# Performance work log

Hardware: AMD Instinct MI355X
Metric: run time of the kernel (lower is better)

The kernel has to match this reference:

```python
import jax, jax.numpy as jnp
import numpy as np

B, L, H, W = 4, 5000, 256, 256
C_IN, DIM_LOI, N_PTS0, N_PTS1, DIM_FC, N_OUT_LINE = 256, 128, 32, 8, 1024, 2500
SCALE = N_PTS0 // N_PTS1  # MaxPool1d kernel/stride


def setup_inputs() -> dict:
    key = jax.random.key(0)
    ks = jax.random.split(key, 8)
    feature = jax.random.normal(ks[0], (B, C_IN, H, W), jnp.float32)
    # line endpoints in pixel coords of the 256x256 feature map
    lines = jax.random.uniform(ks[1], (B, L, 2, 2), jnp.float32) * (H - 1)
    s = lambda fan: 1.0 / np.sqrt(fan)
    fc1_w = (jax.random.normal(ks[2], (DIM_LOI, C_IN), jnp.float32) * s(C_IN))
    fc1_b = jnp.zeros((DIM_LOI,), jnp.float32)
    w1 = jax.random.normal(ks[3], (DIM_LOI * N_PTS1, DIM_FC), jnp.float32) * s(DIM_LOI * N_PTS1)
    b1 = jnp.zeros((DIM_FC,), jnp.float32)
    w2 = jax.random.normal(ks[4], (DIM_FC, DIM_FC), jnp.float32) * s(DIM_FC)
    b2 = jnp.zeros((DIM_FC,), jnp.float32)
    w3 = jax.random.normal(ks[5], (DIM_FC, 4), jnp.float32) * s(DIM_FC)
    b3 = jnp.zeros((4,), jnp.float32)
    return dict(feature=feature, lines=lines, fc1_w=fc1_w, fc1_b=fc1_b,
                w1=w1, b1=b1, w2=w2, b2=b2, w3=w3, b3=b3)


def reference(feature, lines, fc1_w, fc1_b, w1, b1, w2, b2, w3, b3):
    # fc1: 1x1 conv  [B,C_IN,H,W] -> [B,DIM_LOI,H,W]
    x = jnp.einsum('bchw,oc->bohw', feature, fc1_w) + fc1_b[None, :, None, None]

    # sample N_PTS0 points along each line (lerp between endpoints), minus 0.5
    lam = jnp.linspace(0.0, 1.0, N_PTS0, dtype=feature.dtype)[None, None, :, None]
    p = lines[:, :, 0:1, :] * lam + lines[:, :, 1:2, :] * (1.0 - lam) - 0.5  # [B,L,P,2]
    px, py = p[..., 0], p[..., 1]  # px indexes H (rows), py indexes W (cols)
    px0 = jnp.clip(jnp.floor(px), 0.0, H - 1.0)
    py0 = jnp.clip(jnp.floor(py), 0.0, W - 1.0)
    px1 = jnp.clip(px0 + 1.0, 0.0, H - 1.0)
    py1 = jnp.clip(py0 + 1.0, 0.0, W - 1.0)
    ix0, iy0 = px0.astype(jnp.int32), py0.astype(jnp.int32)
    ix1, iy1 = px1.astype(jnp.int32), py1.astype(jnp.int32)
    idx00 = ix0 * W + iy0
    idx10 = ix1 * W + iy0
    idx01 = ix0 * W + iy1
    idx11 = ix1 * W + iy1
    w00 = (px1 - px) * (py1 - py)
    w10 = (px - px0) * (py1 - py)
    w01 = (px1 - px) * (py - py0)
    w11 = (px - px0) * (py - py0)

    def gather_one(fmap, i00, i10, i01, i11, g00, g10, g01, g11):
        f = fmap.reshape(DIM_LOI, H * W)
        g = lambda idx: f[:, idx.reshape(-1)].reshape(DIM_LOI, L, N_PTS0)
        return g(i00) * g00 + g(i10) * g10 + g(i01) * g01 + g(i11) * g11

    xp = jax.vmap(gather_one)(x, idx00, idx10, idx01, idx11, w00, w10, w01, w11)
    # xp: [B, DIM_LOI, L, N_PTS0] -> maxpool along points -> [B, DIM_LOI, L, N_PTS1]
    xp = xp.reshape(B, DIM_LOI, L, N_PTS1, SCALE).max(-1)
    # reshape like torch: [N, DIM_LOI, N_PTS1] -> [N, DIM_LOI*N_PTS1] (channel-major)
    feat = xp.transpose(0, 2, 1, 3).reshape(B, L, DIM_LOI * N_PTS1)

    # fc2 MLP -> 4 logits
    h = jax.nn.relu(feat @ w1 + b1)
    h = jax.nn.relu(h @ w2 + b2)
    logits = h @ w3 + b3  # [B, L, 4]
    s = jax.nn.softmax(logits, axis=-1)

    # threshold conditions
    keep = ((s[..., 1] > 0.25) | (s[..., 2] > 0.25) | (s[..., 3] > 0.25)) & (s[..., 0] < 0.25)

    def select(p0, s0, m):
        cnt = m.sum()
        key = jnp.where(m, jnp.argmax(s0, -1), -1)  # masked-out get -1 -> sorted last
        order = jnp.argsort(-key)  # stable desc sort of argmax class
        idx = order[jnp.arange(N_OUT_LINE) % jnp.maximum(cnt, 1)]
        lo = jnp.where(cnt > 0, p0[idx], 0.0)
        so = jnp.where(cnt > 0, s0[idx], 0.0)
        return lo, so

    lines_out, score_out = jax.vmap(select)(lines, s, keep)
    return lines_out, score_out, s
```

## Files before the change

kernel.cpp:

```cpp
#include <hip/hip_runtime.h>
#include <cstdint>
#include <cstddef>

#define B_     4
#define L_     5000
#define H_     256
#define W_     256
#define HW_    65536
#define CIN_   256
#define DLOI_  128
#define NPTS0_ 32
#define NPTS1_ 8
#define DFC_   1024
#define NOUT_  2500
#define M_     (B_*L_)
#define MPAD_  20096
#define NBAND_ 157

typedef _Float16 f16;
typedef _Float16 f16x4 __attribute__((ext_vector_type(4)));
typedef _Float16 f16x8 __attribute__((ext_vector_type(8)));
typedef float    f32x4 __attribute__((ext_vector_type(4)));

__device__ __forceinline__ void gload16(const void* g, void* l) {
  __builtin_amdgcn_global_load_lds(
      (const __attribute__((address_space(1))) void*)g,
      (__attribute__((address_space(3))) void*)l, 16, 0, 0);
}

__global__ __launch_bounds__(256) void k_wsplit(const float* __restrict__ src,
                                                f16* __restrict__ h,
                                                f16* __restrict__ l) {
  int i = (blockIdx.x * 256 + threadIdx.x) * 4;
  float4 v = *(const float4*)(src + i);
  f16 h0 = (f16)v.x, h1 = (f16)v.y, h2 = (f16)v.z, h3 = (f16)v.w;
  *(f16x4*)(h + i) = (f16x4){h0, h1, h2, h3};
  *(f16x4*)(l + i) = (f16x4){(f16)(v.x - (float)h0), (f16)(v.y - (float)h1),
                             (f16)(v.z - (float)h2), (f16)(v.w - (float)h3)};
}

__global__ __launch_bounds__(256) void k_conv_mfma(const float* __restrict__ fin,
                                                   const f16* __restrict__ wh,
                                                   const f16* __restrict__ wl,
                                                   const float* __restrict__ bias,
                                                   float* __restrict__ xout) {
  __shared__ f16 lds[16384];
  const int t = threadIdx.x;
  const int P0 = blockIdx.x * 128;
  const int b  = P0 >> 16;
  const int ph0 = P0 & 65535;
  const int lane = t & 63, wave = t >> 6;
  const int quad = lane >> 4, lo = lane & 15;
  const int wm = wave >> 1, wn = wave & 1;

  const int c_base = (t & 7) * 4;
  const int p = (t >> 3) * 4;
  const size_t fbase = (size_t)b * CIN_ * HW_ + (size_t)ph0 + p;

  const int srow = t >> 2;
  const int skb  = (t & 3) * 16;
  const char* gBh = (const char*)wh + (size_t)srow * 512 + skb;
  const char* gBl = (const char*)wl + (size_t)srow * 512 + skb;
  char* ldsB = (char*)lds + t * 16;

  f32x4 acc[4][4];
  #pragma unroll
  for (int mt = 0; mt < 4; mt++)
    #pragma unroll
    for (int nt = 0; nt < 4; nt++) acc[mt][nt] = (f32x4){0.f, 0.f, 0.f, 0.f};

  float4 av[4], nv[4];
  #pragma unroll
  for (int j = 0; j < 4; j++)
    av[j] = *(const float4*)(fin + fbase + (size_t)(c_base + j) * HW_);

  for (int kc = 0; kc < 8; kc++) {
    const size_t bko = (size_t)kc * 64;
    gload16(gBh + bko,         ldsB + 16384);
    gload16(gBh + 32768 + bko, ldsB + 16384 + 4096);
    gload16(gBl + bko,         ldsB + 24576);
    gload16(gBl + 32768 + bko, ldsB + 24576 + 4096);

    #pragma unroll
    for (int i = 0; i < 4; i++) {
      f16 hh[4], ll[4];
      #pragma unroll
      for (int j = 0; j < 4; j++) {
        float v = ((const float*)&av[j])[i];
        hh[j] = (f16)v;
        ll[j] = (f16)(v - (float)hh[j]);
      }
      *(f16x4*)(&lds[(p + i) * 32 + c_base])        = (f16x4){hh[0], hh[1], hh[2], hh[3]};
      *(f16x4*)(&lds[4096 + (p + i) * 32 + c_base]) = (f16x4){ll[0], ll[1], ll[2], ll[3]};
    }
    __syncthreads();

    if (kc < 7) {
      #pragma unroll
      for (int j = 0; j < 4; j++)
        nv[j] = *(const float4*)(fin + fbase + (size_t)((kc + 1) * 32 + c_base + j) * HW_);
    }

    f16x8 ah[4], al[4], bh4[4], bl4[4];
    #pragma unroll
    for (int mt = 0; mt < 4; mt++) {
      int row = wm * 64 + mt * 16 + lo;
      ah[mt] = *(const f16x8*)(&lds[row * 32 + quad * 8]);
      al[mt] = *(const f16x8*)(&lds[4096 + row * 32 + quad * 8]);
    }
    #pragma unroll
    for (int nt = 0; nt < 4; nt++) {
      int row = wn * 64 + nt * 16 + lo;
      bh4[nt] = *(const f16x8*)(&lds[8192 + row * 32 + quad * 8]);
      bl4[nt] = *(const f16x8*)(&lds[12288 + row * 32 + quad * 8]);
    }
    #pragma unroll
    for (int mt = 0; mt < 4; mt++)
      #pragma unroll
      for (int nt = 0; nt < 4; nt++) {
        acc[mt][nt] = __builtin_amdgcn_mfma_f32_16x16x32_f16(ah[mt], bh4[nt], acc[mt][nt], 0, 0, 0);
        acc[mt][nt] = __builtin_amdgcn_mfma_f32_16x16x32_f16(ah[mt], bl4[nt], acc[mt][nt], 0, 0, 0);
        acc[mt][nt] = __builtin_amdgcn_mfma_f32_16x16x32_f16(al[mt], bh4[nt], acc[mt][nt], 0, 0, 0);
      }
    __syncthreads();
    #pragma unroll
    for (int j = 0; j < 4; j++) av[j] = nv[j];
  }

  #pragma unroll
  for (int nt = 0; nt < 4; nt++) {
    int col = wn * 64 + nt * 16 + lo;
    float bv = bias[col];
    #pragma unroll
    for (int mt = 0; mt < 4; mt++) {
      int rowb = P0 + wm * 64 + mt * 16 + quad * 4;
      #pragma unroll
      for (int r = 0; r < 4; r++)
        xout[(size_t)(rowb + r) * DLOI_ + col] = acc[mt][nt][r] + bv;
    }
  }
}

__global__ __launch_bounds__(128) void k_sample(const float* __restrict__ x,
                                                const float* __restrict__ lines,
                                                f16* __restrict__ fh,
                                                f16* __restrict__ fl) {
  const int blk = blockIdx.x;
  const int b = blk / L_;
  const int c = threadIdx.x;
  const float* ln = lines + (size_t)blk * 4;
  const float e0x = ln[0], e0y = ln[1], e1x = ln[2], e1y = ln[3];
  const float* xb = x + (size_t)b * HW_ * DLOI_;
  f16x8 vh, vl;
  for (int q = 0; q < NPTS1_; q++) {
    float m = -1e30f;
    #pragma unroll
    for (int r = 0; r < 4; r++) {
      int i = q * 4 + r;
      float lam = (float)i * (1.0f / 31.0f);
      float px = e0x * lam + e1x * (1.f - lam) - 0.5f;
      float py = e0y * lam + e1y * (1.f - lam) - 0.5f;
      float px0 = fminf(fmaxf(floorf(px), 0.f), 255.f);
      float py0 = fminf(fmaxf(floorf(py), 0.f), 255.f);
      float px1 = fminf(px0 + 1.f, 255.f);
      float py1 = fminf(py0 + 1.f, 255.f);
      int ix0 = (int)px0, iy0 = (int)py0, ix1 = (int)px1, iy1 = (int)py1;
      float w00 = (px1 - px) * (py1 - py);
      float w10 = (px - px0) * (py1 - py);
      float w01 = (px1 - px) * (py - py0);
      float w11 = (px - px0) * (py - py0);
      float v = w00 * xb[(size_t)(ix0 * W_ + iy0) * DLOI_ + c]
              + w10 * xb[(size_t)(ix1 * W_ + iy0) * DLOI_ + c]
              + w01 * xb[(size_t)(ix0 * W_ + iy1) * DLOI_ + c]
              + w11 * xb[(size_t)(ix1 * W_ + iy1) * DLOI_ + c];
      m = fmaxf(m, v);
    }
    f16 h = (f16)m;
    vh[q] = h;
    vl[q] = (f16)(m - (float)h);
  }
  *(f16x8*)(fh + (size_t)blk * DFC_ + c * 8) = vh;
  *(f16x8*)(fl + (size_t)blk * DFC_ + c * 8) = vl;
}

__global__ __launch_bounds__(256) void k_tsplit(const float* __restrict__ Wsrc,
                                                f16* __restrict__ Th,
                                                f16* __restrict__ Tl) {
  __shared__ float tile[32][33];
  const int bj = blockIdx.x, bi = blockIdx.y;
  const int tx = threadIdx.x & 31, ty = threadIdx.x >> 5;
  #pragma unroll
  for (int r = ty; r < 32; r += 8)
    tile[r][tx] = Wsrc[(size_t)(bi * 32 + r) * 1024 + bj * 32 + tx];
  __syncthreads();
  #pragma unroll
  for (int r = ty; r < 32; r += 8) {
    float v = tile[tx][r];
    f16 h = (f16)v;
    size_t o = (size_t)(bj * 32 + r) * 1024 + bi * 32 + tx;
    Th[o] = h;
    Tl[o] = (f16)(v - (float)h);
  }
}

template <bool SPLIT_OUT>
__global__ __launch_bounds__(256) void k_gemm_f16x3(
    const f16* __restrict__ Ah, const f16* __restrict__ Al,
    const f16* __restrict__ Bh, const f16* __restrict__ Bl,
    const float* __restrict__ bias,
    f16* __restrict__ Oh, f16* __restrict__ Ol,
    const float* __restrict__ w3, float* __restrict__ part) {
  constexpr int K = DFC_;
  __shared__ f16 lds[16384];
  const int bid = blockIdx.x;
  const int xcd = bid & 7;
  const int t8  = bid >> 3;
  const int nb  = t8 & 7;
  const int rb  = xcd * 20 + (t8 >> 3);
  if (rb >= NBAND_) return;
  const int n0 = nb * 128;
  const int r0 = rb * 128;
  const int t = threadIdx.x;
  const int lane = t & 63, wave = t >> 6;
  const int quad = lane >> 4, lo = lane & 15;
  const int wm = wave >> 1, wn = wave & 1;

  const int srow = t >> 2;
  const int skb  = (t & 3) * 16;
  const char* gA_h = (const char*)Ah + (size_t)(r0 + srow) * (K * 2) + skb;
  const char* gA_l = (const char*)Al + (size_t)(r0 + srow) * (K * 2) + skb;
  const char* gB_h = (const char*)Bh + (size_t)(n0 + srow) * (K * 2) + skb;
  const char* gB_l = (const char*)Bl + (size_t)(n0 + srow) * (K * 2) + skb;
  char* lb = (char*)lds + t * 16;
  const size_t rstride64 = (size_t)64 * K * 2;

  f32x4 acc[4][4];
  #pragma unroll
  for (int mt = 0; mt < 4; mt++)
    #pragma unroll
    for (int nt = 0; nt < 4; nt++) acc[mt][nt] = (f32x4){0.f, 0.f, 0.f, 0.f};

  for (int kc = 0; kc < K / 32; kc++) {
    const size_t go = (size_t)kc * 64;
    gload16(gA_h + go,             lb);
    gload16(gA_h + rstride64 + go, lb + 4096);
    gload16(gA_l + go,             lb + 8192);
    gload16(gA_l + rstride64 + go, lb + 12288);
    gload16(gB_h + go,             lb + 16384);
    gload16(gB_h + rstride64 + go, lb + 20480);
    gload16(gB_l + go,             lb + 24576);
    gload16(gB_l + rstride64 + go, lb + 28672);
    __syncthreads();

    f16x8 ah[4], al[4], bh[4], bl[4];
    #pragma unroll
    for (int mt = 0; mt < 4; mt++) {
      int row = wm * 64 + mt * 16 + lo;
      ah[mt] = *(const f16x8*)(lds + row * 32 + quad * 8);
      al[mt] = *(const f16x8*)(lds + 4096 + row * 32 + quad * 8);
    }
    #pragma unroll
    for (int nt = 0; nt < 4; nt++) {
      int row = wn * 64 + nt * 16 + lo;
      bh[nt] = *(const f16x8*)(lds + 8192 + row * 32 + quad * 8);
      bl[nt] = *(const f16x8*)(lds + 12288 + row * 32 + quad * 8);
    }
    #pragma unroll
    for (int mt = 0; mt < 4; mt++)
      #pragma unroll
      for (int nt = 0; nt < 4; nt++) {
        acc[mt][nt] = __builtin_amdgcn_mfma_f32_16x16x32_f16(ah[mt], bh[nt], acc[mt][nt], 0, 0, 0);
        acc[mt][nt] = __builtin_amdgcn_mfma_f32_16x16x32_f16(ah[mt], bl[nt], acc[mt][nt], 0, 0, 0);
        acc[mt][nt] = __builtin_amdgcn_mfma_f32_16x16x32_f16(al[mt], bh[nt], acc[mt][nt], 0, 0, 0);
      }
    __syncthreads();
  }

  if (SPLIT_OUT) {
    #pragma unroll
    for (int mt = 0; mt < 4; mt++)
      #pragma unroll
      for (int nt = 0; nt < 4; nt++) {
        int col = n0 + wn * 64 + nt * 16 + lo;
        float bv = bias[col];
        int rowb = r0 + wm * 64 + mt * 16 + quad * 4;
        #pragma unroll
        for (int r = 0; r < 4; r++) {
          int row = rowb + r;
          if (row < M_) {
            float v = fmaxf(acc[mt][nt][r] + bv, 0.f);
            f16 h = (f16)v;
            Oh[(size_t)row * DFC_ + col] = h;
            Ol[(size_t)row * DFC_ + col] = (f16)(v - (float)h);
          }
        }
      }
  } else {
    const int slot = nb * 2 + wn;
    #pragma unroll
    for (int mt = 0; mt < 4; mt++) {
      float p[4][4];
      #pragma unroll
      for (int r = 0; r < 4; r++)
        #pragma unroll
        for (int j = 0; j < 4; j++) p[r][j] = 0.f;
      #pragma unroll
      for (int nt = 0; nt < 4; nt++) {
        int col = n0 + wn * 64 + nt * 16 + lo;
        float bv = bias[col];
        float4 wv = *(const float4*)(w3 + col * 4);
        #pragma unroll
        for (int r = 0; r < 4; r++) {
          float v = fmaxf(acc[mt][nt][r] + bv, 0.f);
          p[r][0] = fmaf(v, wv.x, p[r][0]);
          p[r][1] = fmaf(v, wv.y, p[r][1]);
          p[r][2] = fmaf(v, wv.z, p[r][2]);
          p[r][3] = fmaf(v, wv.w, p[r][3]);
        }
      }
      #pragma unroll
      for (int r = 0; r < 4; r++)
        #pragma unroll
        for (int j = 0; j < 4; j++) {
          p[r][j] += __shfl_xor(p[r][j], 1);
          p[r][j] += __shfl_xor(p[r][j], 2);
          p[r][j] += __shfl_xor(p[r][j], 4);
          p[r][j] += __shfl_xor(p[r][j], 8);
        }
      if (lo == 0) {
        int rowb = r0 + wm * 64 + mt * 16 + quad * 4;
        #pragma unroll
        for (int r = 0; r < 4; r++)
          *(float4*)(part + ((size_t)slot * MPAD_ + rowb + r) * 4) =
              make_float4(p[r][0], p[r][1], p[r][2], p[r][3]);
      }
    }
  }
}

__global__ __launch_bounds__(256) void k_head2(const float* __restrict__ part,
                                               const float* __restrict__ b3,
                                               float* __restrict__ s_out,
                                               int* __restrict__ key_out) {
  const int row = blockIdx.x * 256 + threadIdx.x;
  if (row >= M_) return;
  float l0 = b3[0], l1 = b3[1], l2 = b3[2], l3 = b3[3];
  #pragma unroll
  for (int sl = 0; sl < 16; sl++) {
    float4 p = *(const float4*)(part + ((size_t)sl * MPAD_ + row) * 4);
    l0 += p.x; l1 += p.y; l2 += p.z; l3 += p.w;
  }
  float mx = fmaxf(fmaxf(l0, l1), fmaxf(l2, l3));
  float e0 = expf(l0 - mx), e1 = expf(l1 - mx), e2 = expf(l2 - mx), e3 = expf(l3 - mx);
  float inv = 1.f / (e0 + e1 + e2 + e3);
  float s0 = e0 * inv, s1 = e1 * inv, s2 = e2 * inv, s3 = e3 * inv;
  *(float4*)(s_out + (size_t)row * 4) = make_float4(s0, s1, s2, s3);
  bool keep = ((s1 > 0.25f) || (s2 > 0.25f) || (s3 > 0.25f)) && (s0 < 0.25f);
  int am = 0; float best = s0;
  if (s1 > best) { best = s1; am = 1; }
  if (s2 > best) { best = s2; am = 2; }
  if (s3 > best) { best = s3; am = 3; }
  key_out[row] = keep ? am : -1;
}

__global__ __launch_bounds__(1024) void k_select(const int* __restrict__ key,
                                                 const float* __restrict__ lines,
                                                 const float* __restrict__ s,
                                                 float* __restrict__ out_lines,
                                                 float* __restrict__ out_score) {
  __shared__ int s_ord[L_];
  __shared__ int s_scan[1024];
  __shared__ int s_tot[5];
  const int b = blockIdx.x;
  const int t = threadIdx.x;
  const int base_l = t * 5;
  int cls[5];
  int c[5] = {0, 0, 0, 0, 0};
  #pragma unroll
  for (int i = 0; i < 5; i++) {
    int l = base_l + i;
    int cl = -1;
    if (l < L_) {
      int k = key[b * L_ + l];
      cl = (k < 0) ? 4 : (3 - k);
      c[cl]++;
    }
    cls[i] = cl;
  }
  int pf[5];
  for (int cc = 0; cc < 5; cc++) {
    s_scan[t] = c[cc];
    __syncthreads();
    for (int off = 1; off < 1024; off <<= 1) {
      int add = (t >= off) ? s_scan[t - off] : 0;
      __syncthreads();
      s_scan[t] += add;
      __syncthreads();
    }
    pf[cc] = s_scan[t] - c[cc];
    if (t == 1023) s_tot[cc] = s_scan[1023];
    __syncthreads();
  }
  int basec[5];
  basec[0] = 0;
  #pragma unroll
  for (int cc = 1; cc < 5; cc++) basec[cc] = basec[cc - 1] + s_tot[cc - 1];
  int run[5] = {0, 0, 0, 0, 0};
  #pragma unroll
  for (int i = 0; i < 5; i++) {
    if (cls[i] >= 0) {
      int cl = cls[i];
      int pos = basec[cl] + pf[cl] + run[cl];
      run[cl]++;
      s_ord[pos] = base_l + i;
    }
  }
  const int cnt = L_ - s_tot[4];
  __syncthreads();
  for (int j = t; j < NOUT_; j += 1024) {
    float4 lv = make_float4(0.f, 0.f, 0.f, 0.f);
    float4 sv = make_float4(0.f, 0.f, 0.f, 0.f);
    if (cnt > 0) {
      int idx = s_ord[j % cnt];
      lv = *(const float4*)(lines + (size_t)(b * L_ + idx) * 4);
      sv = *(const float4*)(s + (size_t)(b * L_ + idx) * 4);
    }
    *(float4*)(out_lines + (size_t)(b * NOUT_ + j) * 4) = lv;
    *(float4*)(out_score + (size_t)(b * NOUT_ + j) * 4) = sv;
  }
}

extern "C" void kernel_launch(void* const* d_in, const int* in_sizes, int n_in,
                              void* d_out, int out_size, void* d_ws, size_t ws_size,
                              hipStream_t stream) {
  const float* feature = (const float*)d_in[0];
  const float* lines   = (const float*)d_in[1];
  const float* fc1_w   = (const float*)d_in[2];
  const float* fc1_b   = (const float*)d_in[3];
  const float* w1      = (const float*)d_in[4];
  const float* b1      = (const float*)d_in[5];
  const float* w2      = (const float*)d_in[6];
  const float* b2      = (const float*)d_in[7];
  const float* w3      = (const float*)d_in[8];
  const float* b3      = (const float*)d_in[9];

  float* out_lines = (float*)d_out;
  float* out_score = out_lines + B_ * NOUT_ * 4;
  float* s_out     = out_score + B_ * NOUT_ * 4;

  char* ws = (char*)d_ws;
  float* x    = (float*)(ws);
  f16*   h1h  = (f16*)(ws);
  f16*   h1l  = (f16*)(ws + 41156608ull);
  float* part = (float*)(ws + 82313216ull);
  f16*   fh   = (f16*)(ws + 134217728ull);
  f16*   fl   = (f16*)(ws + 134217728ull + 41156608ull);
  f16*   wt1h = (f16*)(ws + 216530944ull);
  f16*   wt1l = (f16*)(ws + 216530944ull + 2097152ull);
  f16*   wt2h = (f16*)(ws + 216530944ull + 2ull * 2097152ull);
  f16*   wt2l = (f16*)(ws + 216530944ull + 3ull * 2097152ull);
  int*   keys = (int*)(ws + 224919552ull);
  f16*   wc_h = (f16*)(ws + 224999552ull);
  f16*   wc_l = (f16*)(ws + 224999552ull + 65536ull);

  k_wsplit<<<dim3(32), 256, 0, stream>>>(fc1_w, wc_h, wc_l);
  k_tsplit<<<dim3(32, 32), 256, 0, stream>>>(w1, wt1h, wt1l);
  k_tsplit<<<dim3(32, 32), 256, 0, stream>>>(w2, wt2h, wt2l);
  k_conv_mfma<<<dim3((B_ * HW_) / 128), 256, 0, stream>>>(feature, wc_h, wc_l, fc1_b, x);
  k_sample<<<dim3(M_), 128, 0, stream>>>(x, lines, fh, fl);
  k_gemm_f16x3<true><<<dim3(1280), 256, 0, stream>>>(
      fh, fl, wt1h, wt1l, b1, h1h, h1l, nullptr, nullptr);
  k_gemm_f16x3<false><<<dim3(1280), 256, 0, stream>>>(
      h1h, h1l, wt2h, wt2l, b2, nullptr, nullptr, w3, part);
  k_head2<<<dim3((M_ + 255) / 256), 256, 0, stream>>>(part, b3, s_out, keys);
  k_select<<<dim3(B_), 1024, 0, stream>>>(keys, lines, s_out, out_lines, out_score);
}
```

Baseline: 906.3 us.

## Restructure split-f16 GEMM into triple-buffered 128x256 tile pipeline with swizzled LDS

The two MLP GEMMs switch from 128x128 tiles with 256 threads and a single synchronous LDS buffer to 128x256 tiles with 512 threads. Three LDS stages let global loads for step k+2 overlap the MFMA work on the current step. Each K-step is split into three MFMA phases (hi*hi, lo*hi, hi*lo), with loads interleaved between phases, wave priority raised during MFMAs, and an XOR swizzle on LDS rows to reduce bank conflicts. Blocks are remapped contiguously per XCD, and the partial-logit slot indexing is adjusted to the new wave layout. The 144KB of LDS allows only one workgroup per CU, and the hand-placed waitcnt and barrier sequence is fragile.

```diff
diff --git a/kernel.cpp b/kernel.cpp
--- a/kernel.cpp
+++ b/kernel.cpp
@@ -203,36 +203,69 @@
   }
 }
 
+#define BKT_    32
+#define NTT_    (DFC_/BKT_)
+#define SLOT_B_ 49152
+#define AH_O_   0
+#define AL_O_   8192
+#define BH_O_   16384
+#define BL_O_   32768
+
 template <bool SPLIT_OUT>
-__global__ __launch_bounds__(256) void k_gemm_f16x3(
+__global__ __launch_bounds__(512, 2) void k_gemm_f16x3(
     const f16* __restrict__ Ah, const f16* __restrict__ Al,
     const f16* __restrict__ Bh, const f16* __restrict__ Bl,
     const float* __restrict__ bias,
     f16* __restrict__ Oh, f16* __restrict__ Ol,
     const float* __restrict__ w3, float* __restrict__ part) {
-  constexpr int K = DFC_;
-  __shared__ f16 lds[16384];
-  const int bid = blockIdx.x;
-  const int xcd = bid & 7;
-  const int t8  = bid >> 3;
-  const int nb  = t8 & 7;
-  const int rb  = xcd * 20 + (t8 >> 3);
-  if (rb >= NBAND_) return;
-  const int n0 = nb * 128;
-  const int r0 = rb * 128;
+  __shared__ f16 lds[3 * SLOT_B_ / 2];
+  char* ldsc = (char*)lds;
+
+  const int orig = blockIdx.x;
+  const int xcd = orig & 7, bidx = orig >> 3;
+  const int qq = 628 >> 3, rr = 628 & 7;
+  const int wg = (xcd < rr ? xcd * (qq + 1) : rr * (qq + 1) + (xcd - rr) * qq) + bidx;
+  const int band = wg >> 2;
+  const int nb   = wg & 3;
+  const int r0 = band * 128;
+  const int n0 = nb * 256;
+
   const int t = threadIdx.x;
   const int lane = t & 63, wave = t >> 6;
   const int quad = lane >> 4, lo = lane & 15;
-  const int wm = wave >> 1, wn = wave & 1;
-
-  const int srow = t >> 2;
-  const int skb  = (t & 3) * 16;
-  const char* gA_h = (const char*)Ah + (size_t)(r0 + srow) * (K * 2) + skb;
-  const char* gA_l = (const char*)Al + (size_t)(r0 + srow) * (K * 2) + skb;
-  const char* gB_h = (const char*)Bh + (size_t)(n0 + srow) * (K * 2) + skb;
-  const char* gB_l = (const char*)Bl + (size_t)(n0 + srow) * (K * 2) + skb;
-  char* lb = (char*)lds + t * 16;
-  const size_t rstride64 = (size_t)64 * K * 2;
+  const int wm = wave >> 2, wn = wave & 3;
+
+  const uint32_t usA  = (uint32_t)t ^ (((uint32_t)t >> 3) & 7);
+  const uint32_t uB1  = (uint32_t)t + 512u;
+  const uint32_t usB1 = uB1 ^ ((uB1 >> 3) & 7);
+  const size_t sA  = (size_t)(usA  >> 2) * 2048 + (size_t)(usA  & 3) * 16;
+  const size_t sB1 = (size_t)(usB1 >> 2) * 2048 + (size_t)(usB1 & 3) * 16;
+
+  const char* gAh  = (const char*)Ah + (size_t)r0 * 2048 + sA;
+  const char* gAl  = (const char*)Al + (size_t)r0 * 2048 + sA;
+  const char* gBh0 = (const char*)Bh + (size_t)n0 * 2048 + sA;
+  const char* gBh1 = (const char*)Bh + (size_t)n0 * 2048 + sB1;
+  const char* gBl0 = (const char*)Bl + (size_t)n0 * 2048 + sA;
+  const char* gBl1 = (const char*)Bl + (size_t)n0 * 2048 + sB1;
+
+  const int dAh  = AH_O_ + t * 16;
+  const int dAl  = AL_O_ + t * 16;
+  const int dBh0 = BH_O_ + t * 16;
+  const int dBh1 = BH_O_ + 8192 + t * 16;
+  const int dBl0 = BL_O_ + t * 16;
+  const int dBl1 = BL_O_ + 8192 + t * 16;
+
+  int roffA[4], roffB[4];
+  #pragma unroll
+  for (int mt = 0; mt < 4; mt++) {
+    int r = wm * 64 + mt * 16 + lo;
+    roffA[mt] = (((r * 4 + quad) ^ ((r >> 1) & 7)) << 4);
+  }
+  #pragma unroll
+  for (int nt = 0; nt < 4; nt++) {
+    int r = wn * 64 + nt * 16 + lo;
+    roffB[nt] = (((r * 4 + quad) ^ ((r >> 1) & 7)) << 4);
+  }
 
   f32x4 acc[4][4];
   #pragma unroll
@@ -240,53 +273,98 @@
     #pragma unroll
     for (int nt = 0; nt < 4; nt++) acc[mt][nt] = (f32x4){0.f, 0.f, 0.f, 0.f};
 
-  for (int kc = 0; kc < K / 32; kc++) {
-    const size_t go = (size_t)kc * 64;
-    gload16(gA_h + go,             lb);
-    gload16(gA_h + rstride64 + go, lb + 4096);
-    gload16(gA_l + go,             lb + 8192);
-    gload16(gA_l + rstride64 + go, lb + 12288);
-    gload16(gB_h + go,             lb + 16384);
-    gload16(gB_h + rstride64 + go, lb + 20480);
-    gload16(gB_l + go,             lb + 24576);
-    gload16(gB_l + rstride64 + go, lb + 28672);
-    __syncthreads();
+  gload16(gAh,        ldsc + dAh);
+  gload16(gAl,        ldsc + dAl);
+  gload16(gBh0,       ldsc + dBh0);
+  gload16(gBh1,       ldsc + dBh1);
+  gload16(gBl0,       ldsc + dBl0);
+  gload16(gBl1,       ldsc + dBl1);
+  gload16(gAh  + 64,  ldsc + SLOT_B_ + dAh);
+  gload16(gAl  + 64,  ldsc + SLOT_B_ + dAl);
+  gload16(gBh0 + 64,  ldsc + SLOT_B_ + dBh0);
+  gload16(gBh1 + 64,  ldsc + SLOT_B_ + dBh1);
+  gload16(gBl0 + 64,  ldsc + SLOT_B_ + dBl0);
+  gload16(gBl1 + 64,  ldsc + SLOT_B_ + dBl1);
+  asm volatile("s_waitcnt vmcnt(6)" ::: "memory");
+  __builtin_amdgcn_s_barrier();
+
+  int cur = 0, stg = 2;
+  for (int tt = 0; tt < NTT_; ++tt) {
+    const char* sc = ldsc + cur * SLOT_B_;
+    char* sw = ldsc + stg * SLOT_B_;
+    const size_t go = (size_t)tt * 64 + 128;
+    const bool pf = (tt + 2 < NTT_);
 
     f16x8 ah[4], al[4], bh[4], bl[4];
-    #pragma unroll
-    for (int mt = 0; mt < 4; mt++) {
-      int row = wm * 64 + mt * 16 + lo;
-      ah[mt] = *(const f16x8*)(lds + row * 32 + quad * 8);
-      al[mt] = *(const f16x8*)(lds + 4096 + row * 32 + quad * 8);
-    }
+
+    #pragma unroll
+    for (int mt = 0; mt < 4; mt++)
+      ah[mt] = *(const f16x8*)(sc + AH_O_ + roffA[mt]);
+    #pragma unroll
+    for (int nt = 0; nt < 4; nt++)
+      bh[nt] = *(const f16x8*)(sc + BH_O_ + roffB[nt]);
+    if (pf) { gload16(gAh + go, sw + dAh); gload16(gAl + go, sw + dAl); }
+    __builtin_amdgcn_s_barrier();
+    asm volatile("s_waitcnt lgkmcnt(0)" ::: "memory");
+    __builtin_amdgcn_sched_barrier(0);
+    __builtin_amdgcn_s_setprio(1);
+    #pragma unroll
+    for (int mt = 0; mt < 4; mt++)
+      #pragma unroll
+      for (int nt = 0; nt < 4; nt++)
+        acc[mt][nt] = __builtin_amdgcn_mfma_f32_16x16x32_f16(ah[mt], bh[nt], acc[mt][nt], 0, 0, 0);
+    __builtin_amdgcn_s_setprio(0);
+    __builtin_amdgcn_s_barrier();
+
+    #pragma unroll
+    for (int mt = 0; mt < 4; mt++)
+      al[mt] = *(const f16x8*)(sc + AL_O_ + roffA[mt]);
+    if (pf) { gload16(gBh0 + go, sw + dBh0); gload16(gBh1 + go, sw + dBh1); }
+    __builtin_amdgcn_s_barrier();
+    asm volatile("s_waitcnt lgkmcnt(0)" ::: "memory");
+    __builtin_amdgcn_sched_barrier(0);
+    __builtin_amdgcn_s_setprio(1);
+    #pragma unroll
+    for (int mt = 0; mt < 4; mt++)
+      #pragma unroll
+      for (int nt = 0; nt < 4; nt++)
+        acc[mt][nt] = __builtin_amdgcn_mfma_f32_16x16x32_f16(al[mt], bh[nt], acc[mt][nt], 0, 0, 0);
+    __builtin_amdgcn_s_setprio(0);
+    __builtin_amdgcn_s_barrier();
+
+    #pragma unroll
+    for (int nt = 0; nt < 4; nt++)
+      bl[nt] = *(const f16x8*)(sc + BL_O_ + roffB[nt]);
+    if (pf) { gload16(gBl0 + go, sw + dBl0); gload16(gBl1 + go, sw + dBl1); }
+    __builtin_amdgcn_s_barrier();
+    asm volatile("s_waitcnt lgkmcnt(0)" ::: "memory");
+    __builtin_amdgcn_sched_barrier(0);
+    __builtin_amdgcn_s_setprio(1);
+    #pragma unroll
+    for (int mt = 0; mt < 4; mt++)
+      #pragma unroll
+      for (int nt = 0; nt < 4; nt++)
+        acc[mt][nt] = __builtin_amdgcn_mfma_f32_16x16x32_f16(ah[mt], bl[nt], acc[mt][nt], 0, 0, 0);
+    __builtin_amdgcn_s_setprio(0);
+    if (tt < NTT_ - 2) asm volatile("s_waitcnt vmcnt(6)" ::: "memory");
+    else               asm volatile("s_waitcnt vmcnt(0)" ::: "memory");
+    __builtin_amdgcn_s_barrier();
+
+    cur = (cur == 2) ? 0 : cur + 1;
+    stg = (stg == 2) ? 0 : stg + 1;
+  }
+
+  if (SPLIT_OUT) {
     #pragma unroll
     for (int nt = 0; nt < 4; nt++) {
-      int row = wn * 64 + nt * 16 + lo;
-      bh[nt] = *(const f16x8*)(lds + 8192 + row * 32 + quad * 8);
-      bl[nt] = *(const f16x8*)(lds + 12288 + row * 32 + quad * 8);
-    }
-    #pragma unroll
-    for (int mt = 0; mt < 4; mt++)
-      #pragma unroll
-      for (int nt = 0; nt < 4; nt++) {
-        acc[mt][nt] = __builtin_amdgcn_mfma_f32_16x16x32_f16(ah[mt], bh[nt], acc[mt][nt], 0, 0, 0);
-        acc[mt][nt] = __builtin_amdgcn_mfma_f32_16x16x32_f16(ah[mt], bl[nt], acc[mt][nt], 0, 0, 0);
-        acc[mt][nt] = __builtin_amdgcn_mfma_f32_16x16x32_f16(al[mt], bh[nt], acc[mt][nt], 0, 0, 0);
-      }
-    __syncthreads();
-  }
-
-  if (SPLIT_OUT) {
-    #pragma unroll
-    for (int mt = 0; mt < 4; mt++)
-      #pragma unroll
-      for (int nt = 0; nt < 4; nt++) {
-        int col = n0 + wn * 64 + nt * 16 + lo;
-        float bv = bias[col];
-        int rowb = r0 + wm * 64 + mt * 16 + quad * 4;
+      const int col = n0 + wn * 64 + nt * 16 + lo;
+      const float bv = bias[col];
+      #pragma unroll
+      for (int mt = 0; mt < 4; mt++) {
+        const int rowb = r0 + wm * 64 + mt * 16 + quad * 4;
         #pragma unroll
         for (int r = 0; r < 4; r++) {
-          int row = rowb + r;
+          const int row = rowb + r;
           if (row < M_) {
             float v = fmaxf(acc[mt][nt][r] + bv, 0.f);
             f16 h = (f16)v;
@@ -295,8 +373,9 @@
           }
         }
       }
+    }
   } else {
-    const int slot = nb * 2 + wn;
+    const int slot = nb * 4 + wn;
     #pragma unroll
     for (int mt = 0; mt < 4; mt++) {
       float p[4][4];
@@ -306,8 +385,8 @@
         for (int j = 0; j < 4; j++) p[r][j] = 0.f;
       #pragma unroll
       for (int nt = 0; nt < 4; nt++) {
-        int col = n0 + wn * 64 + nt * 16 + lo;
-        float bv = bias[col];
+        const int col = n0 + wn * 64 + nt * 16 + lo;
+        const float bv = bias[col];
         float4 wv = *(const float4*)(w3 + col * 4);
         #pragma unroll
         for (int r = 0; r < 4; r++) {
@@ -328,7 +407,7 @@
           p[r][j] += __shfl_xor(p[r][j], 8);
         }
       if (lo == 0) {
-        int rowb = r0 + wm * 64 + mt * 16 + quad * 4;
+        const int rowb = r0 + wm * 64 + mt * 16 + quad * 4;
         #pragma unroll
         for (int r = 0; r < 4; r++)
           *(float4*)(part + ((size_t)slot * MPAD_ + rowb + r) * 4) =
@@ -468,9 +547,9 @@
   k_tsplit<<<dim3(32, 32), 256, 0, stream>>>(w2, wt2h, wt2l);
   k_conv_mfma<<<dim3((B_ * HW_) / 128), 256, 0, stream>>>(feature, wc_h, wc_l, fc1_b, x);
   k_sample<<<dim3(M_), 128, 0, stream>>>(x, lines, fh, fl);
-  k_gemm_f16x3<true><<<dim3(1280), 256, 0, stream>>>(
+  k_gemm_f16x3<true><<<dim3(628), 512, 0, stream>>>(
       fh, fl, wt1h, wt1l, b1, h1h, h1l, nullptr, nullptr);
-  k_gemm_f16x3<false><<<dim3(1280), 256, 0, stream>>>(
+  k_gemm_f16x3<false><<<dim3(628), 512, 0, stream>>>(
       h1h, h1l, wt2h, wt2l, b2, nullptr, nullptr, w3, part);
   k_head2<<<dim3((M_ + 255) / 256), 256, 0, stream>>>(part, b3, s_out, keys);
   k_select<<<dim3(B_), 1024, 0, stream>>>(keys, lines, s_out, out_lines, out_score);
```

Result: no change. 895.8 us (-1.2%).
